# Kernel tuning notes

Hardware: AMD Instinct MI355X
Metric: run time of the kernel (lower is better)

The kernel has to match this reference:

```python
import jax, jax.numpy as jnp
import numpy as np

B, LQ, LKV = 32, 512, 512
SIZE, H = 512, 8
HD = SIZE // H
SCALE = 1.0 / np.sqrt(HD)
LN_EPS = 1e-5


def layer_norm(x, w, b):
    mu = jnp.mean(x, axis=-1, keepdims=True)
    var = jnp.mean(jnp.square(x - mu), axis=-1, keepdims=True)
    return (x - mu) * jax.lax.rsqrt(var + LN_EPS) * w + b


def setup_inputs() -> dict:
    key = jax.random.key(0)
    ks = jax.random.split(key, 8)
    s = 0.02
    return {
        "query": jax.random.normal(ks[0], (B, LQ, SIZE), jnp.float32),
        "key_value": jax.random.normal(ks[1], (B, LKV, SIZE), jnp.float32),
        "Wq": jax.random.normal(ks[2], (SIZE, SIZE), jnp.float32) * s,
        "bq": jnp.zeros((SIZE,), jnp.float32),
        "Wk": jax.random.normal(ks[3], (SIZE, SIZE), jnp.float32) * s,
        "bk": jnp.zeros((SIZE,), jnp.float32),
        "Wv": jax.random.normal(ks[4], (SIZE, SIZE), jnp.float32) * s,
        "bv": jnp.zeros((SIZE,), jnp.float32),
        "Wo": jax.random.normal(ks[5], (SIZE, SIZE), jnp.float32) * s,
        "bo": jnp.zeros((SIZE,), jnp.float32),
        "ln0_w": jnp.ones((SIZE,), jnp.float32),
        "ln0_b": jnp.zeros((SIZE,), jnp.float32),
        "ln1_w": jnp.ones((SIZE,), jnp.float32),
        "ln1_b": jnp.zeros((SIZE,), jnp.float32),
    }


def reference(query, key_value, Wq, bq, Wk, bk, Wv, bv, Wo, bo, ln0_w, ln0_b, ln1_w, ln1_b):
    b, lq, _ = query.shape
    lkv = key_value.shape[1]
    # projections
    q = query @ Wq.T + bq          # [B, Lq, SIZE]
    k = key_value @ Wk.T + bk      # [B, Lkv, SIZE]
    v = key_value @ Wv.T + bv
    # split heads: torch cat(split(head_size, 2), 0) == [B,L,H,HD] view with head axis separate
    qh = q.reshape(b, lq, H, HD)
    kh = k.reshape(b, lkv, H, HD)
    vh = v.reshape(b, lkv, H, HD)
    # attention scores [B, H, Lq, Lkv]
    A_ = jnp.einsum("bqhd,bkhd->bhqk", qh, kh) * SCALE
    # signed softmax: tanh(A_) * softmax(sqrt(A_^2 + 0.01)) over keys
    A = jnp.tanh(A_) * jax.nn.softmax(jnp.sqrt(jnp.square(A_) + 0.01), axis=-1)
    # residual q + attention output, merge heads back
    oh = qh + jnp.einsum("bhqk,bkhd->bqhd", A, vh)   # [B, Lq, H, HD]
    output = oh.reshape(b, lq, SIZE)
    output = layer_norm(output, ln0_w, ln0_b)
    output = output + jax.nn.relu(output @ Wo.T + bo)
    output = layer_norm(output, ln1_w, ln1_b)
    return output
```

## Files before the change

kernel.cpp:

```cpp
#include <hip/hip_runtime.h>

#define SIZE_D 512
#define HEADS  8
#define HDIM   64
#define BATCH  32
#define SEQ    512
#define SCALE_F 0.125f
#define NROWS  (BATCH * SEQ)

typedef __attribute__((ext_vector_type(8))) short bf16x8;
typedef __attribute__((ext_vector_type(4))) float f32x4;
typedef __attribute__((ext_vector_type(4))) unsigned int u32x4;

__device__ __forceinline__ unsigned short f2bf(float f) {
    union { float f; unsigned int u; } c{f};
    unsigned int x = c.u;
    x += 0x7fffu + ((x >> 16) & 1u);
    return (unsigned short)(x >> 16);
}
__device__ __forceinline__ float bf2f(unsigned short u) {
    union { unsigned int i; float f; } c;
    c.i = (unsigned int)u << 16;
    return c.f;
}
__device__ __forceinline__ void gload_lds16(const unsigned short* g, unsigned short* l) {
    __builtin_amdgcn_global_load_lds(
        (const __attribute__((address_space(1))) unsigned int*)g,
        (__attribute__((address_space(3))) unsigned int*)l, 16, 0, 0);
}

__global__ __launch_bounds__(256) void cvt_act(const float* __restrict__ q,
                                               const float* __restrict__ kv,
                                               unsigned short* __restrict__ dq,
                                               unsigned short* __restrict__ dkv) {
    const float* s = blockIdx.y ? kv : q;
    unsigned short* d = blockIdx.y ? dkv : dq;
    const int n = NROWS * SIZE_D;
    const int stride = gridDim.x * blockDim.x * 4;
    for (int i = (blockIdx.x * blockDim.x + threadIdx.x) * 4; i < n; i += stride) {
        const float4 v = *reinterpret_cast<const float4*>(s + i);
        ushort4 o;
        o.x = f2bf(v.x); o.y = f2bf(v.y); o.z = f2bf(v.z); o.w = f2bf(v.w);
        *reinterpret_cast<ushort4*>(d + i) = o;
    }
}

__global__ __launch_bounds__(256) void cvt_w4(const float* __restrict__ w0,
                                              const float* __restrict__ w1,
                                              const float* __restrict__ w2,
                                              const float* __restrict__ w3,
                                              unsigned short* __restrict__ d) {
    const float* srcs[4] = {w0, w1, w2, w3};
    const float* s = srcs[blockIdx.y];
    unsigned short* dst = d + (size_t)blockIdx.y * (SIZE_D * SIZE_D);
    const int n = SIZE_D * SIZE_D;
    const int stride = gridDim.x * blockDim.x * 4;
    for (int i = (blockIdx.x * blockDim.x + threadIdx.x) * 4; i < n; i += stride) {
        const float4 v = *reinterpret_cast<const float4*>(s + i);
        ushort4 o;
        o.x = f2bf(v.x); o.y = f2bf(v.y); o.z = f2bf(v.z); o.w = f2bf(v.w);
        *reinterpret_cast<ushort4*>(dst + i) = o;
    }
}

template <int KV>
__global__ __launch_bounds__(256, 2) void gemm_proj(const unsigned short* __restrict__ A,
                                                    const unsigned short* __restrict__ W,
                                                    const float* __restrict__ bias0,
                                                    const float* __restrict__ bias1,
                                                    unsigned short* __restrict__ D0,
                                                    unsigned short* __restrict__ D1) {
    __shared__ __align__(16) unsigned short Ad[2][128 * 64];
    __shared__ __align__(16) unsigned short Bd[2][128 * 64];

    const int tid  = threadIdx.x;
    const int wv   = tid >> 6;
    const int lane = tid & 63;
    const int bm   = blockIdx.x * 128;
    const int bn   = blockIdx.y * 128;
    const int wr   = wv >> 1;
    const int wc   = wv & 1;

    auto stage = [&](int buf, int t) {
        const int k0 = t * 64;
#pragma unroll
        for (int i = 0; i < 4; ++i) {
            const int o     = (wv * 32 + i * 8) * 128 + lane * 16;
            const int row   = o >> 7;
            const int inrow = (o & 127) ^ ((row & 7) << 4);
            const int col   = inrow >> 1;
            gload_lds16(A + (size_t)(bm + row) * SIZE_D + k0 + col, &Ad[buf][o >> 1]);
            gload_lds16(W + (size_t)(bn + row) * SIZE_D + k0 + col, &Bd[buf][o >> 1]);
        }
    };

    f32x4 acc[4][4];
#pragma unroll
    for (int mt = 0; mt < 4; ++mt)
#pragma unroll
        for (int nt = 0; nt < 4; ++nt) acc[mt][nt] = (f32x4){0.f, 0.f, 0.f, 0.f};

    stage(0, 0);
    __syncthreads();
    int cur = 0;

    for (int t = 0; t < 8; ++t) {
        if (t < 7) stage(cur ^ 1, t + 1);

        bf16x8 af[2][4], bfr[2][4];
#pragma unroll
        for (int kc = 0; kc < 2; ++kc) {
#pragma unroll
            for (int mt = 0; mt < 4; ++mt) {
                const int r = wr * 64 + mt * 16 + (lane & 15);
                int byte = r * 128 + kc * 64 + (lane >> 4) * 16;
                byte ^= (r & 7) << 4;
                af[kc][mt] = *reinterpret_cast<const bf16x8*>(
                    reinterpret_cast<const char*>(&Ad[cur][0]) + byte);
            }
#pragma unroll
            for (int nt = 0; nt < 4; ++nt) {
                const int r = wc * 64 + nt * 16 + (lane & 15);
                int byte = r * 128 + kc * 64 + (lane >> 4) * 16;
                byte ^= (r & 7) << 4;
                bfr[kc][nt] = *reinterpret_cast<const bf16x8*>(
                    reinterpret_cast<const char*>(&Bd[cur][0]) + byte);
            }
        }
#pragma unroll
        for (int kc = 0; kc < 2; ++kc)
#pragma unroll
            for (int mt = 0; mt < 4; ++mt)
#pragma unroll
                for (int nt = 0; nt < 4; ++nt)
                    acc[mt][nt] = __builtin_amdgcn_mfma_f32_16x16x32_bf16(
                        af[kc][mt], bfr[kc][nt], acc[mt][nt], 0, 0, 0);

        __syncthreads();
        cur ^= 1;
    }

    if (KV == 0 || bn < 512) {
#pragma unroll
        for (int nt = 0; nt < 4; ++nt) {
            const int col = bn + wc * 64 + nt * 16 + (lane & 15);
            const float bc = bias0[col];
            const int h = (col >> 6) & 7, dd = col & 63;
#pragma unroll
            for (int mt = 0; mt < 4; ++mt) {
                const int row0 = bm + wr * 64 + mt * 16 + (lane >> 4) * 4;
#pragma unroll
                for (int r = 0; r < 4; ++r) {
                    const int row = row0 + r;
                    const int b_ = row >> 9, l = row & 511;
                    float z = acc[mt][nt][r] + bc;
                    if (KV) z *= SCALE_F;
                    D0[(((size_t)b_ * HEADS + h) * SEQ + l) * HDIM + dd] = f2bf(z);
                }
            }
        }
    } else {
#pragma unroll
        for (int nt = 0; nt < 4; ++nt) {
            const int c2 = bn + wc * 64 + nt * 16 + (lane & 15) - 512;
            const float bc = bias1[c2];
            const int hV = c2 >> 6, dV = c2 & 63;
#pragma unroll
            for (int mt = 0; mt < 4; ++mt) {
                const int row0 = bm + wr * 64 + mt * 16 + (lane >> 4) * 4;
                const int b_ = row0 >> 9, kv = row0 & 511;
                ushort4 pk;
                pk.x = f2bf(acc[mt][nt][0] + bc);
                pk.y = f2bf(acc[mt][nt][1] + bc);
                pk.z = f2bf(acc[mt][nt][2] + bc);
                pk.w = f2bf(acc[mt][nt][3] + bc);
                *reinterpret_cast<ushort4*>(
                    &D1[(((size_t)b_ * HEADS + hV) * HDIM + dV) * SEQ + kv]) = pk;
            }
        }
    }
}

__global__ __launch_bounds__(256, 2) void attn_mfma(const unsigned short* __restrict__ Qh,
                                                    const unsigned short* __restrict__ Kh,
                                                    const unsigned short* __restrict__ Vt,
                                                    float* __restrict__ outq) {
    __shared__ __align__(16) unsigned short WL[4][64 * 64];

    const int tid  = threadIdx.x;
    const int wv   = tid >> 6;
    const int lane = tid & 63;
    const int bh   = blockIdx.x;
    const int half = blockIdx.y;
    const int b    = bh >> 3;
    const int h    = bh & 7;

    const unsigned short* Qb = Qh + (size_t)bh * (SEQ * HDIM);
    const unsigned short* Kb = Kh + (size_t)bh * (SEQ * HDIM);
    const unsigned short* Vb = Vt + (size_t)bh * (HDIM * SEQ);

    const int m0 = half * 256 + wv * 64;

    bf16x8 qf[4][2];
#pragma unroll
    for (int mt = 0; mt < 4; ++mt)
#pragma unroll
        for (int kc = 0; kc < 2; ++kc) {
            const int m = m0 + mt * 16 + (lane & 15);
            union { u32x4 u; bf16x8 v; } cv;
            cv.u = *reinterpret_cast<const u32x4*>(
                Qb + (size_t)m * HDIM + kc * 32 + (lane >> 4) * 8);
            qf[mt][kc] = cv.v;
        }

    unsigned short* myW = &WL[wv][0];
    f32x4 oacc[4][4];
    float esum[4] = {0.f, 0.f, 0.f, 0.f};
#pragma unroll
    for (int mt = 0; mt < 4; ++mt)
#pragma unroll
        for (int x = 0; x < 4; ++x) oacc[mt][x] = (f32x4){0.f, 0.f, 0.f, 0.f};

    for (int t = 0; t < 8; ++t) {
        const int kv0 = t * 64;
        f32x4 sacc[4][4];
#pragma unroll
        for (int nt = 0; nt < 4; ++nt)
#pragma unroll
            for (int mt = 0; mt < 4; ++mt) sacc[nt][mt] = (f32x4){0.f, 0.f, 0.f, 0.f};

#pragma unroll
        for (int kc = 0; kc < 2; ++kc) {
            bf16x8 kf[4];
#pragma unroll
            for (int nt = 0; nt < 4; ++nt) {
                const int kv = kv0 + nt * 16 + (lane & 15);
                union { u32x4 u; bf16x8 v; } cv;
                cv.u = *reinterpret_cast<const u32x4*>(
                    Kb + (size_t)kv * HDIM + kc * 32 + (lane >> 4) * 8);
                kf[nt] = cv.v;
            }
#pragma unroll
            for (int nt = 0; nt < 4; ++nt)
#pragma unroll
                for (int mt = 0; mt < 4; ++mt)
                    sacc[nt][mt] = __builtin_amdgcn_mfma_f32_16x16x32_bf16(
                        kf[nt], qf[mt][kc], sacc[nt][mt], 0, 0, 0);
        }

#pragma unroll
        for (int nt = 0; nt < 4; ++nt)
#pragma unroll
            for (int mt = 0; mt < 4; ++mt) {
                float w[4];
#pragma unroll
                for (int r = 0; r < 4; ++r) {
                    const float s  = sacc[nt][mt][r];
                    const float a  = fminf(fabsf(s), 30.0f);
                    const float tt = __expf(a);
                    const float t2 = tt * tt;
                    const float u  = __builtin_amdgcn_sqrtf(fmaf(s, s, 0.01f));
                    const float dl = u - a;
                    const float ed = fmaf(dl, fmaf(dl, fmaf(dl, 0.16666667f, 0.5f), 1.0f), 1.0f);
                    const float eu = tt * ed;
                    esum[mt] += eu;
                    const float th = (t2 - 1.0f) * __builtin_amdgcn_rcpf(t2 + 1.0f);
                    w[r] = __builtin_copysignf(th * eu, s);
                }
                uint2 pk;
                pk.x = (__float_as_uint(w[1]) & 0xffff0000u) | (__float_as_uint(w[0]) >> 16);
                pk.y = (__float_as_uint(w[3]) & 0xffff0000u) | (__float_as_uint(w[2]) >> 16);
                int byte = (mt * 16 + (lane & 15)) * 128 + nt * 32 + (lane >> 4) * 8;
                byte ^= (lane & 7) << 4;
                *reinterpret_cast<uint2*>(reinterpret_cast<char*>(myW) + byte) = pk;
            }

#pragma unroll
        for (int kc2 = 0; kc2 < 2; ++kc2) {
            bf16x8 wf[4], vf[4];
#pragma unroll
            for (int mt = 0; mt < 4; ++mt) {
                const int row = mt * 16 + (lane & 15);
                int byte = row * 128 + kc2 * 64 + (lane >> 4) * 16;
                byte ^= (row & 7) << 4;
                union { u32x4 u; bf16x8 v; } cv;
                cv.u = *reinterpret_cast<const u32x4*>(reinterpret_cast<char*>(myW) + byte);
                wf[mt] = cv.v;
            }
#pragma unroll
            for (int dt = 0; dt < 4; ++dt) {
                const int d = dt * 16 + (lane & 15);
                union { u32x4 u; bf16x8 v; } cv;
                cv.u = *reinterpret_cast<const u32x4*>(
                    Vb + (size_t)d * SEQ + kv0 + kc2 * 32 + (lane >> 4) * 8);
                vf[dt] = cv.v;
            }
#pragma unroll
            for (int mt = 0; mt < 4; ++mt)
#pragma unroll
                for (int dt = 0; dt < 4; ++dt)
                    oacc[mt][dt] = __builtin_amdgcn_mfma_f32_16x16x32_bf16(
                        wf[mt], vf[dt], oacc[mt][dt], 0, 0, 0);
        }
    }

    float rden[4];
#pragma unroll
    for (int mt = 0; mt < 4; ++mt) {
        float e = esum[mt];
        e += __shfl_xor(e, 16);
        e += __shfl_xor(e, 32);
        rden[mt] = __builtin_amdgcn_rcpf(e);
    }
    float rr_[4][4];
#pragma unroll
    for (int mt = 0; mt < 4; ++mt)
#pragma unroll
        for (int r = 0; r < 4; ++r)
            rr_[mt][r] = __shfl(rden[mt], (lane >> 4) * 4 + r);

#pragma unroll
    for (int mt = 0; mt < 4; ++mt)
#pragma unroll
        for (int dt = 0; dt < 4; ++dt)
#pragma unroll
            for (int r = 0; r < 4; ++r) {
                const int m = m0 + mt * 16 + (lane >> 4) * 4 + r;
                const int d = dt * 16 + (lane & 15);
                const float qv = bf2f(Qb[(size_t)m * HDIM + d]);
                outq[((size_t)b * SEQ + m) * SIZE_D + h * HDIM + d] =
                    qv + oacc[mt][dt][r] * rr_[mt][r];
            }
}

__global__ __launch_bounds__(256) void ln0_bf16(const float* __restrict__ in,
                                                const float* __restrict__ w,
                                                const float* __restrict__ b,
                                                unsigned short* __restrict__ outb) {
    const int row = blockIdx.x;
    const int tid = threadIdx.x;
    const float2 x = *reinterpret_cast<const float2*>(&in[(size_t)row * SIZE_D + tid * 2]);

    float s  = x.x + x.y;
    float sq = x.x * x.x + x.y * x.y;
#pragma unroll
    for (int off = 32; off > 0; off >>= 1) {
        s  += __shfl_xor(s, off);
        sq += __shfl_xor(sq, off);
    }
    __shared__ float rs[4], rq[4];
    const int wv = tid >> 6;
    if ((tid & 63) == 0) { rs[wv] = s; rq[wv] = sq; }
    __syncthreads();
    s  = rs[0] + rs[1] + rs[2] + rs[3];
    sq = rq[0] + rq[1] + rq[2] + rq[3];

    const float mu  = s * (1.0f / SIZE_D);
    const float var = sq * (1.0f / SIZE_D) - mu * mu;
    const float rr  = rsqrtf(var + 1e-5f);

    const float2 wv2 = *reinterpret_cast<const float2*>(&w[tid * 2]);
    const float2 bv2 = *reinterpret_cast<const float2*>(&b[tid * 2]);
    ushort2 ob;
    ob.x = f2bf((x.x - mu) * rr * wv2.x + bv2.x);
    ob.y = f2bf((x.y - mu) * rr * wv2.y + bv2.y);
    *reinterpret_cast<ushort2*>(&outb[(size_t)row * SIZE_D + tid * 2]) = ob;
}

__global__ __launch_bounds__(512, 2) void oproj_ln(const unsigned short* __restrict__ X,
                                                   const unsigned short* __restrict__ W,
                                                   const float* __restrict__ bo,
                                                   const float* __restrict__ g1,
                                                   const float* __restrict__ b1,
                                                   float* __restrict__ out) {
    __shared__ __align__(16) unsigned short Ad[2][64 * 64];
    __shared__ __align__(16) unsigned short Bd[2][512 * 64];
    __shared__ float red[64][8][2];
    __shared__ float stat[64][2];

    const int tid  = threadIdx.x;
    const int wv   = tid >> 6;
    const int lane = tid & 63;
    const int bm   = blockIdx.x * 64;

    auto stage = [&](int buf, int t) {
        const int k0 = t * 64;
        {
            const int o     = tid * 16;
            const int row   = o >> 7;
            const int inrow = (o & 127) ^ ((row & 7) << 4);
            const int col   = inrow >> 1;
            gload_lds16(X + (size_t)(bm + row) * SIZE_D + k0 + col, &Ad[buf][o >> 1]);
        }
#pragma unroll
        for (int i = 0; i < 8; ++i) {
            const int o     = i * 8192 + tid * 16;
            const int row   = o >> 7;
            const int inrow = (o & 127) ^ ((row & 7) << 4);
            const int col   = inrow >> 1;
            gload_lds16(W + (size_t)row * SIZE_D + k0 + col, &Bd[buf][o >> 1]);
        }
    };

    f32x4 acc[4][4];
#pragma unroll
    for (int mt = 0; mt < 4; ++mt)
#pragma unroll
        for (int nt = 0; nt < 4; ++nt) acc[mt][nt] = (f32x4){0.f, 0.f, 0.f, 0.f};

    stage(0, 0);
    __syncthreads();
    int cur = 0;

    for (int t = 0; t < 8; ++t) {
        if (t < 7) stage(cur ^ 1, t + 1);

        bf16x8 af[2][4], bfr[2][4];
#pragma unroll
        for (int kc = 0; kc < 2; ++kc) {
#pragma unroll
            for (int mt = 0; mt < 4; ++mt) {
                const int r = mt * 16 + (lane & 15);
                int byte = r * 128 + kc * 64 + (lane >> 4) * 16;
                byte ^= (r & 7) << 4;
                af[kc][mt] = *reinterpret_cast<const bf16x8*>(
                    reinterpret_cast<const char*>(&Ad[cur][0]) + byte);
            }
#pragma unroll
            for (int nt = 0; nt < 4; ++nt) {
                const int r = wv * 64 + nt * 16 + (lane & 15);
                int byte = r * 128 + kc * 64 + (lane >> 4) * 16;
                byte ^= (r & 7) << 4;
                bfr[kc][nt] = *reinterpret_cast<const bf16x8*>(
                    reinterpret_cast<const char*>(&Bd[cur][0]) + byte);
            }
        }
#pragma unroll
        for (int kc = 0; kc < 2; ++kc)
#pragma unroll
            for (int mt = 0; mt < 4; ++mt)
#pragma unroll
                for (int nt = 0; nt < 4; ++nt)
                    acc[mt][nt] = __builtin_amdgcn_mfma_f32_16x16x32_bf16(
                        af[kc][mt], bfr[kc][nt], acc[mt][nt], 0, 0, 0);

        __syncthreads();
        cur ^= 1;
    }

#pragma unroll
    for (int nt = 0; nt < 4; ++nt) {
        const int n  = wv * 64 + nt * 16 + (lane & 15);
        const float bc = bo[n];
#pragma unroll
        for (int mt = 0; mt < 4; ++mt) {
            const int row0 = bm + mt * 16 + (lane >> 4) * 4;
#pragma unroll
            for (int r = 0; r < 4; ++r) {
                const float R = bf2f(X[(size_t)(row0 + r) * SIZE_D + n]);
                acc[mt][nt][r] = R + fmaxf(acc[mt][nt][r] + bc, 0.0f);
            }
        }
    }

    float ps[4][4], pq[4][4];
#pragma unroll
    for (int mt = 0; mt < 4; ++mt)
#pragma unroll
        for (int r = 0; r < 4; ++r) {
            float s = 0.f, q = 0.f;
#pragma unroll
            for (int nt = 0; nt < 4; ++nt) {
                const float v = acc[mt][nt][r];
                s += v; q += v * v;
            }
#pragma unroll
            for (int off = 1; off <= 8; off <<= 1) {
                s += __shfl_xor(s, off);
                q += __shfl_xor(q, off);
            }
            ps[mt][r] = s; pq[mt][r] = q;
        }
    {
        const int mtw = (lane & 15) >> 2, rw = lane & 3;
        const int rowL = mtw * 16 + (lane >> 4) * 4 + rw;
        red[rowL][wv][0] = ps[mtw][rw];
        red[rowL][wv][1] = pq[mtw][rw];
    }
    __syncthreads();
    if (tid < 64) {
        float s = 0.f, q = 0.f;
#pragma unroll
        for (int w8 = 0; w8 < 8; ++w8) { s += red[tid][w8][0]; q += red[tid][w8][1]; }
        const float mu  = s * (1.0f / SIZE_D);
        const float var = q * (1.0f / SIZE_D) - mu * mu;
        stat[tid][0] = mu;
        stat[tid][1] = rsqrtf(var + 1e-5f);
    }
    __syncthreads();

#pragma unroll
    for (int nt = 0; nt < 4; ++nt) {
        const int n = wv * 64 + nt * 16 + (lane & 15);
        const float g = g1[n], bb = b1[n];
#pragma unroll
        for (int mt = 0; mt < 4; ++mt) {
#pragma unroll
            for (int r = 0; r < 4; ++r) {
                const int rowL = mt * 16 + (lane >> 4) * 4 + r;
                const float y = (acc[mt][nt][r] - stat[rowL][0]) * stat[rowL][1];
                out[(size_t)(bm + rowL) * SIZE_D + n] = y * g + bb;
            }
        }
    }
}

extern "C" void kernel_launch(void* const* d_in, const int* in_sizes, int n_in,
                              void* d_out, int out_size, void* d_ws, size_t ws_size,
                              hipStream_t stream) {
    const float* query = (const float*)d_in[0];
    const float* keyv  = (const float*)d_in[1];
    const float* Wq    = (const float*)d_in[2];
    const float* bq    = (const float*)d_in[3];
    const float* Wk    = (const float*)d_in[4];
    const float* bk    = (const float*)d_in[5];
    const float* Wv    = (const float*)d_in[6];
    const float* bv    = (const float*)d_in[7];
    const float* Wo    = (const float*)d_in[8];
    const float* bo    = (const float*)d_in[9];
    const float* ln0w  = (const float*)d_in[10];
    const float* ln0b  = (const float*)d_in[11];
    const float* ln1w  = (const float*)d_in[12];
    const float* ln1b  = (const float*)d_in[13];
    float* out = (float*)d_out;

    char* ws = (char*)d_ws;
    unsigned short* Qbf  = (unsigned short*)ws;
    unsigned short* KVbf = (unsigned short*)(ws + ((size_t)16 << 20));
    float*          qbuf = (float*)ws;
    unsigned short* Qh   = (unsigned short*)(ws + ((size_t)32 << 20));
    unsigned short* Xbf  = Qh;
    unsigned short* Kh   = (unsigned short*)(ws + ((size_t)48 << 20));
    unsigned short* Vt   = (unsigned short*)(ws + ((size_t)64 << 20));
    unsigned short* Wbf  = (unsigned short*)(ws + ((size_t)80 << 20));
    unsigned short* WqB  = Wbf;
    unsigned short* WkB  = Wbf + 262144;
    unsigned short* WoB  = Wbf + 786432;

    cvt_act<<<dim3(1024, 2), 256, 0, stream>>>(query, keyv, Qbf, KVbf);
    cvt_w4<<<dim3(64, 4), 256, 0, stream>>>(Wq, Wk, Wv, Wo, Wbf);

    gemm_proj<0><<<dim3(128, 4), 256, 0, stream>>>(Qbf, WqB, bq, nullptr, Qh, nullptr);
    gemm_proj<1><<<dim3(128, 8), 256, 0, stream>>>(KVbf, WkB, bk, bv, Kh, Vt);

    attn_mfma<<<dim3(BATCH * HEADS, 2), 256, 0, stream>>>(Qh, Kh, Vt, qbuf);

    ln0_bf16<<<NROWS, 256, 0, stream>>>(qbuf, ln0w, ln0b, Xbf);

    oproj_ln<<<NROWS / 64, 512, 0, stream>>>(Xbf, WoB, bo, ln1w, ln1b, out);
}
```

Measured before the change: 171.7 us.

## Merge Q/K/V projections into one launch, stage K/V in LDS, shrink oproj K-tile

The separate Q and KV projection GEMM launches are merged into one 12-column-block launch that picks its input and output by blockIdx.y. This removes one launch and lets all blocks run in a single wave. The attention kernel now double-buffers swizzled K and V tiles into shared memory with async loads, where before each wave read them directly from global memory. The output-projection kernel halves its K-tile to 32 with a new swizzle, cutting LDS use at the cost of twice as many iterations and barriers.

```diff
diff --git a/kernel.cpp b/kernel.cpp
--- a/kernel.cpp
+++ b/kernel.cpp
@@ -63,23 +63,28 @@
     }
 }
 
-template <int KV>
-__global__ __launch_bounds__(256, 2) void gemm_proj(const unsigned short* __restrict__ A,
-                                                    const unsigned short* __restrict__ W,
-                                                    const float* __restrict__ bias0,
-                                                    const float* __restrict__ bias1,
-                                                    unsigned short* __restrict__ D0,
-                                                    unsigned short* __restrict__ D1) {
+__global__ __launch_bounds__(256, 2) void gemm_proj3(const unsigned short* __restrict__ Qbf,
+                                                     const unsigned short* __restrict__ KVbf,
+                                                     const unsigned short* __restrict__ Wall,
+                                                     const float* __restrict__ bq,
+                                                     const float* __restrict__ bk,
+                                                     const float* __restrict__ bv,
+                                                     unsigned short* __restrict__ Qh,
+                                                     unsigned short* __restrict__ Kh,
+                                                     unsigned short* __restrict__ Vt) {
     __shared__ __align__(16) unsigned short Ad[2][128 * 64];
     __shared__ __align__(16) unsigned short Bd[2][128 * 64];
 
     const int tid  = threadIdx.x;
     const int wv   = tid >> 6;
     const int lane = tid & 63;
+    const int y    = blockIdx.y;
     const int bm   = blockIdx.x * 128;
-    const int bn   = blockIdx.y * 128;
+    const int bn   = y * 128;
     const int wr   = wv >> 1;
     const int wc   = wv & 1;
+
+    const unsigned short* A = (y < 4) ? Qbf : KVbf;
 
     auto stage = [&](int buf, int t) {
         const int k0 = t * 64;
@@ -90,7 +95,7 @@
             const int inrow = (o & 127) ^ ((row & 7) << 4);
             const int col   = inrow >> 1;
             gload_lds16(A + (size_t)(bm + row) * SIZE_D + k0 + col, &Ad[buf][o >> 1]);
-            gload_lds16(W + (size_t)(bn + row) * SIZE_D + k0 + col, &Bd[buf][o >> 1]);
+            gload_lds16(Wall + (size_t)(bn + row) * SIZE_D + k0 + col, &Bd[buf][o >> 1]);
         }
     };
 
@@ -140,12 +145,15 @@
         cur ^= 1;
     }
 
-    if (KV == 0 || bn < 512) {
+    if (y < 8) {
+        const float* bias = (y < 4) ? bq : bk;
+        unsigned short* D = (y < 4) ? Qh : Kh;
+        const int coff = (y < 4) ? 0 : 512;
 #pragma unroll
         for (int nt = 0; nt < 4; ++nt) {
-            const int col = bn + wc * 64 + nt * 16 + (lane & 15);
-            const float bc = bias0[col];
-            const int h = (col >> 6) & 7, dd = col & 63;
+            const int colL = bn - coff + wc * 64 + nt * 16 + (lane & 15);
+            const float bc = bias[colL];
+            const int h = colL >> 6, dd = colL & 63;
 #pragma unroll
             for (int mt = 0; mt < 4; ++mt) {
                 const int row0 = bm + wr * 64 + mt * 16 + (lane >> 4) * 4;
@@ -154,16 +162,16 @@
                     const int row = row0 + r;
                     const int b_ = row >> 9, l = row & 511;
                     float z = acc[mt][nt][r] + bc;
-                    if (KV) z *= SCALE_F;
-                    D0[(((size_t)b_ * HEADS + h) * SEQ + l) * HDIM + dd] = f2bf(z);
+                    if (y >= 4) z *= SCALE_F;
+                    D[(((size_t)b_ * HEADS + h) * SEQ + l) * HDIM + dd] = f2bf(z);
                 }
             }
         }
     } else {
 #pragma unroll
         for (int nt = 0; nt < 4; ++nt) {
-            const int c2 = bn + wc * 64 + nt * 16 + (lane & 15) - 512;
-            const float bc = bias1[c2];
+            const int c2 = bn - 1024 + wc * 64 + nt * 16 + (lane & 15);
+            const float bc = bv[c2];
             const int hV = c2 >> 6, dV = c2 & 63;
 #pragma unroll
             for (int mt = 0; mt < 4; ++mt) {
@@ -175,7 +183,7 @@
                 pk.z = f2bf(acc[mt][nt][2] + bc);
                 pk.w = f2bf(acc[mt][nt][3] + bc);
                 *reinterpret_cast<ushort4*>(
-                    &D1[(((size_t)b_ * HEADS + hV) * HDIM + dV) * SEQ + kv]) = pk;
+                    &Vt[(((size_t)b_ * HEADS + hV) * HDIM + dV) * SEQ + kv]) = pk;
             }
         }
     }
@@ -185,6 +193,8 @@
                                                     const unsigned short* __restrict__ Kh,
                                                     const unsigned short* __restrict__ Vt,
                                                     float* __restrict__ outq) {
+    __shared__ __align__(16) unsigned short Kt[2][64 * 64];
+    __shared__ __align__(16) unsigned short Vs[2][64 * 64];
     __shared__ __align__(16) unsigned short WL[4][64 * 64];
 
     const int tid  = threadIdx.x;
@@ -201,6 +211,18 @@
 
     const int m0 = half * 256 + wv * 64;
 
+    auto stageKV = [&](int buf, int t) {
+        const int kv0 = t * 64;
+#pragma unroll
+        for (int i = 0; i < 2; ++i) {
+            const int o   = i * 4096 + tid * 16;
+            const int row = o >> 7;
+            const int in  = (o & 127) ^ ((row & 7) << 4);
+            gload_lds16(Kb + (size_t)(kv0 + row) * HDIM + (in >> 1), &Kt[buf][o >> 1]);
+            gload_lds16(Vb + (size_t)row * SEQ + kv0 + (in >> 1), &Vs[buf][o >> 1]);
+        }
+    };
+
     bf16x8 qf[4][2];
 #pragma unroll
     for (int mt = 0; mt < 4; ++mt)
@@ -221,8 +243,13 @@
 #pragma unroll
         for (int x = 0; x < 4; ++x) oacc[mt][x] = (f32x4){0.f, 0.f, 0.f, 0.f};
 
+    stageKV(0, 0);
+    __syncthreads();
+    int cur = 0;
+
     for (int t = 0; t < 8; ++t) {
-        const int kv0 = t * 64;
+        if (t < 7) stageKV(cur ^ 1, t + 1);
+
         f32x4 sacc[4][4];
 #pragma unroll
         for (int nt = 0; nt < 4; ++nt)
@@ -234,11 +261,11 @@
             bf16x8 kf[4];
 #pragma unroll
             for (int nt = 0; nt < 4; ++nt) {
-                const int kv = kv0 + nt * 16 + (lane & 15);
-                union { u32x4 u; bf16x8 v; } cv;
-                cv.u = *reinterpret_cast<const u32x4*>(
-                    Kb + (size_t)kv * HDIM + kc * 32 + (lane >> 4) * 8);
-                kf[nt] = cv.v;
+                const int kvl = nt * 16 + (lane & 15);
+                int byte = kvl * 128 + kc * 64 + (lane >> 4) * 16;
+                byte ^= (kvl & 7) << 4;
+                kf[nt] = *reinterpret_cast<const bf16x8*>(
+                    reinterpret_cast<const char*>(&Kt[cur][0]) + byte);
             }
 #pragma unroll
             for (int nt = 0; nt < 4; ++nt)
@@ -283,17 +310,16 @@
                 const int row = mt * 16 + (lane & 15);
                 int byte = row * 128 + kc2 * 64 + (lane >> 4) * 16;
                 byte ^= (row & 7) << 4;
-                union { u32x4 u; bf16x8 v; } cv;
-                cv.u = *reinterpret_cast<const u32x4*>(reinterpret_cast<char*>(myW) + byte);
-                wf[mt] = cv.v;
+                wf[mt] = *reinterpret_cast<const bf16x8*>(
+                    reinterpret_cast<const char*>(myW) + byte);
             }
 #pragma unroll
             for (int dt = 0; dt < 4; ++dt) {
                 const int d = dt * 16 + (lane & 15);
-                union { u32x4 u; bf16x8 v; } cv;
-                cv.u = *reinterpret_cast<const u32x4*>(
-                    Vb + (size_t)d * SEQ + kv0 + kc2 * 32 + (lane >> 4) * 8);
-                vf[dt] = cv.v;
+                int byte = d * 128 + kc2 * 64 + (lane >> 4) * 16;
+                byte ^= (d & 7) << 4;
+                vf[dt] = *reinterpret_cast<const bf16x8*>(
+                    reinterpret_cast<const char*>(&Vs[cur][0]) + byte);
             }
 #pragma unroll
             for (int mt = 0; mt < 4; ++mt)
@@ -302,6 +328,9 @@
                     oacc[mt][dt] = __builtin_amdgcn_mfma_f32_16x16x32_bf16(
                         wf[mt], vf[dt], oacc[mt][dt], 0, 0, 0);
         }
+
+        __syncthreads();
+        cur ^= 1;
     }
 
     float rden[4];
@@ -373,8 +402,8 @@
                                                    const float* __restrict__ g1,
                                                    const float* __restrict__ b1,
                                                    float* __restrict__ out) {
-    __shared__ __align__(16) unsigned short Ad[2][64 * 64];
-    __shared__ __align__(16) unsigned short Bd[2][512 * 64];
+    __shared__ __align__(16) unsigned short Ad[2][64 * 32];
+    __shared__ __align__(16) unsigned short Bd[2][512 * 32];
     __shared__ float red[64][8][2];
     __shared__ float stat[64][2];
 
@@ -384,21 +413,19 @@
     const int bm   = blockIdx.x * 64;
 
     auto stage = [&](int buf, int t) {
-        const int k0 = t * 64;
-        {
-            const int o     = tid * 16;
-            const int row   = o >> 7;
-            const int inrow = (o & 127) ^ ((row & 7) << 4);
-            const int col   = inrow >> 1;
-            gload_lds16(X + (size_t)(bm + row) * SIZE_D + k0 + col, &Ad[buf][o >> 1]);
-        }
-#pragma unroll
-        for (int i = 0; i < 8; ++i) {
-            const int o     = i * 8192 + tid * 16;
-            const int row   = o >> 7;
-            const int inrow = (o & 127) ^ ((row & 7) << 4);
-            const int col   = inrow >> 1;
-            gload_lds16(W + (size_t)row * SIZE_D + k0 + col, &Bd[buf][o >> 1]);
+        const int k0 = t * 32;
+        if (tid < 256) {
+            const int o   = tid * 16;
+            const int row = o >> 6;
+            const int in  = (o & 63) ^ (((row >> 1) & 3) << 4);
+            gload_lds16(X + (size_t)(bm + row) * SIZE_D + k0 + (in >> 1), &Ad[buf][o >> 1]);
+        }
+#pragma unroll
+        for (int i = 0; i < 4; ++i) {
+            const int o   = i * 8192 + tid * 16;
+            const int row = o >> 6;
+            const int in  = (o & 63) ^ (((row >> 1) & 3) << 4);
+            gload_lds16(W + (size_t)row * SIZE_D + k0 + (in >> 1), &Bd[buf][o >> 1]);
         }
     };
 
@@ -412,37 +439,32 @@
     __syncthreads();
     int cur = 0;
 
-    for (int t = 0; t < 8; ++t) {
-        if (t < 7) stage(cur ^ 1, t + 1);
-
-        bf16x8 af[2][4], bfr[2][4];
-#pragma unroll
-        for (int kc = 0; kc < 2; ++kc) {
-#pragma unroll
-            for (int mt = 0; mt < 4; ++mt) {
-                const int r = mt * 16 + (lane & 15);
-                int byte = r * 128 + kc * 64 + (lane >> 4) * 16;
-                byte ^= (r & 7) << 4;
-                af[kc][mt] = *reinterpret_cast<const bf16x8*>(
-                    reinterpret_cast<const char*>(&Ad[cur][0]) + byte);
-            }
-#pragma unroll
-            for (int nt = 0; nt < 4; ++nt) {
-                const int r = wv * 64 + nt * 16 + (lane & 15);
-                int byte = r * 128 + kc * 64 + (lane >> 4) * 16;
-                byte ^= (r & 7) << 4;
-                bfr[kc][nt] = *reinterpret_cast<const bf16x8*>(
-                    reinterpret_cast<const char*>(&Bd[cur][0]) + byte);
-            }
-        }
-#pragma unroll
-        for (int kc = 0; kc < 2; ++kc)
-#pragma unroll
-            for (int mt = 0; mt < 4; ++mt)
-#pragma unroll
-                for (int nt = 0; nt < 4; ++nt)
-                    acc[mt][nt] = __builtin_amdgcn_mfma_f32_16x16x32_bf16(
-                        af[kc][mt], bfr[kc][nt], acc[mt][nt], 0, 0, 0);
+    for (int t = 0; t < 16; ++t) {
+        if (t < 15) stage(cur ^ 1, t + 1);
+
+        bf16x8 af[4], bfr[4];
+#pragma unroll
+        for (int mt = 0; mt < 4; ++mt) {
+            const int r = mt * 16 + (lane & 15);
+            int byte = r * 64 + (lane >> 4) * 16;
+            byte ^= ((r >> 1) & 3) << 4;
+            af[mt] = *reinterpret_cast<const bf16x8*>(
+                reinterpret_cast<const char*>(&Ad[cur][0]) + byte);
+        }
+#pragma unroll
+        for (int nt = 0; nt < 4; ++nt) {
+            const int r = wv * 64 + nt * 16 + (lane & 15);
+            int byte = r * 64 + (lane >> 4) * 16;
+            byte ^= ((r >> 1) & 3) << 4;
+            bfr[nt] = *reinterpret_cast<const bf16x8*>(
+                reinterpret_cast<const char*>(&Bd[cur][0]) + byte);
+        }
+#pragma unroll
+        for (int mt = 0; mt < 4; ++mt)
+#pragma unroll
+            for (int nt = 0; nt < 4; ++nt)
+                acc[mt][nt] = __builtin_amdgcn_mfma_f32_16x16x32_bf16(
+                    af[mt], bfr[nt], acc[mt][nt], 0, 0, 0);
 
         __syncthreads();
         cur ^= 1;
@@ -543,15 +565,12 @@
     unsigned short* Kh   = (unsigned short*)(ws + ((size_t)48 << 20));
     unsigned short* Vt   = (unsigned short*)(ws + ((size_t)64 << 20));
     unsigned short* Wbf  = (unsigned short*)(ws + ((size_t)80 << 20));
-    unsigned short* WqB  = Wbf;
-    unsigned short* WkB  = Wbf + 262144;
     unsigned short* WoB  = Wbf + 786432;
 
     cvt_act<<<dim3(1024, 2), 256, 0, stream>>>(query, keyv, Qbf, KVbf);
     cvt_w4<<<dim3(64, 4), 256, 0, stream>>>(Wq, Wk, Wv, Wo, Wbf);
 
-    gemm_proj<0><<<dim3(128, 4), 256, 0, stream>>>(Qbf, WqB, bq, nullptr, Qh, nullptr);
-    gemm_proj<1><<<dim3(128, 8), 256, 0, stream>>>(KVbf, WkB, bk, bv, Kh, Vt);
+    gemm_proj3<<<dim3(128, 12), 256, 0, stream>>>(Qbf, KVbf, Wbf, bq, bk, bv, Qh, Kh, Vt);
 
     attn_mfma<<<dim3(BATCH * HEADS, 2), 256, 0, stream>>>(Qh, Kh, Vt, qbuf);
 
```

Result: faster. 168.0 us (-2.2%).
